# Kernel optimization log

Hardware: AMD Instinct MI355X
Metric: run time of the kernel (lower is better)

Reference implementation:

```python
import jax, jax.numpy as jnp
from jax import lax
import numpy as np

EPSILON = 0.1
MAX_ITERS = 20
N, K, D = 16384, 1024, 512


def setup_inputs() -> dict:
    key = jax.random.key(0)
    kx, kp = jax.random.split(key)
    x = jax.random.normal(kx, (N, D), dtype=jnp.float32)
    p = jax.random.normal(kp, (K, D), dtype=jnp.float32)
    return {"x": x, "p": p}


def reference(x, p):
    # Squared-euclidean cost matrix C: [N, K]
    dist_x = jnp.sum(x * x, axis=1, keepdims=True)          # [N, 1]
    dist_p = jnp.sum(p * p, axis=1, keepdims=True).T         # [1, K]
    C = dist_x + dist_p - 2.0 * (x @ p.T)                    # [N, K]
    C = C / (C.max() + 1e-8)
    K_eps = jnp.exp(-C / EPSILON)                            # [N, K]

    n, k = x.shape[0], p.shape[0]
    mu = jnp.full((n,), 1.0 / n, dtype=x.dtype)
    nu = jnp.full((k,), 1.0 / k, dtype=x.dtype)

    def step(carry, _):
        u, v = carry
        u = mu / (K_eps @ v + 1e-8)
        v = nu / (K_eps.T @ u + 1e-8)
        return (u, v), None

    init = (jnp.ones((n,), x.dtype), jnp.ones((k,), x.dtype))
    (u, v), _ = lax.scan(step, init, None, length=MAX_ITERS)

    T_star = u[:, None] * K_eps * v[None, :]                 # [N, K]
    ot_loss = jnp.sum(T_star * C)
    return (T_star, ot_loss)
```

## Files before the change

### kernel.cpp

```cpp
#include <hip/hip_runtime.h>
#include <hip/hip_fp16.h>
#include <cstddef>
#include <cstdint>

#define N_PTS 16384
#define K_PTS 1024
#define D_DIM 512
#define EPS_F 0.1f
#define ITERS 20
#define MU_F (1.0f/16384.0f)
#define NU_F (1.0f/1024.0f)
#define NCOPY 8
#define SINK_BLOCKS 256
#define FLAG_STRIDE 16
#define ACC_TOTAL ((ITERS + 1) * NCOPY * K_PTS)

#define WS_ACCUM_BYTES ((size_t)ACC_TOTAL * 4)
#define WS_FLAGS_BYTES ((size_t)SINK_BLOCKS * FLAG_STRIDE * 4)


typedef float f32x4 __attribute__((ext_vector_type(4)));
typedef _Float16 f16x8 __attribute__((ext_vector_type(8)));

__device__ __forceinline__ float wave_reduce_sum(float s) {
#pragma unroll
  for (int off = 32; off > 0; off >>= 1) s += __shfl_xor(s, off, 64);
  return s;
}
__device__ __forceinline__ float wave_reduce_max(float s) {
#pragma unroll
  for (int off = 32; off > 0; off >>= 1) s = fmaxf(s, __shfl_xor(s, off, 64));
  return s;
}

__device__ __forceinline__ void gl16(const void* g, void* l) {
  __builtin_amdgcn_global_load_lds(
      (const __attribute__((address_space(1))) unsigned int*)g,
      (__attribute__((address_space(3))) unsigned int*)l, 16, 0, 0);
}

__global__ __launch_bounds__(256) void init_kernel(float* __restrict__ accum,
                                                   unsigned int* __restrict__ flags,
                                                   unsigned int* __restrict__ maxbits,
                                                   float* __restrict__ loss) {
  int i = blockIdx.x * 256 + threadIdx.x;
  if (i < ACC_TOTAL) accum[i] = 0.0f;
  if (i < SINK_BLOCKS * FLAG_STRIDE) flags[i] = 0u;
  if (i == 0) { *maxbits = 0u; *loss = 0.0f; }
}

__global__ __launch_bounds__(256) void convert_kernel(const float* __restrict__ X,
                                                      const float* __restrict__ P,
                                                      unsigned short* __restrict__ Xf,
                                                      unsigned short* __restrict__ Pf,
                                                      float* __restrict__ xn,
                                                      float* __restrict__ pn) {
  const int gw = (blockIdx.x * 256 + threadIdx.x) >> 6;
  const int lane = threadIdx.x & 63;

  const float* src;
  unsigned short* dst;
  float* nrm;
  if (gw < N_PTS) {
    src = X + (size_t)gw * D_DIM;
    dst = Xf + (size_t)gw * D_DIM;
    nrm = xn + gw;
  } else {
    int r = gw - N_PTS;
    src = P + (size_t)r * D_DIM;
    dst = Pf + (size_t)r * D_DIM;
    nrm = pn + r;
  }

  float4 f0 = *(const float4*)(src + lane * 8);
  float4 f1 = *(const float4*)(src + lane * 8 + 4);
  float f[8] = {f0.x, f0.y, f0.z, f0.w, f1.x, f1.y, f1.z, f1.w};

  float s = 0.f;
#pragma unroll
  for (int j = 0; j < 8; j++) s += f[j] * f[j];

  unsigned int u[4];
#pragma unroll
  for (int j = 0; j < 4; j++) {
    unsigned int lo = (unsigned int)__half_as_ushort(__float2half(f[2 * j]));
    unsigned int hi = (unsigned int)__half_as_ushort(__float2half(f[2 * j + 1]));
    u[j] = lo | (hi << 16);
  }
  *(uint4*)(dst + lane * 8) = make_uint4(u[0], u[1], u[2], u[3]);

  s = wave_reduce_sum(s);
  if (lane == 0) *nrm = s;
}

__global__ __launch_bounds__(256, 2) void gemm3_kernel(const unsigned short* __restrict__ Xf,
                                                       const unsigned short* __restrict__ Pf,
                                                       const float* __restrict__ xn,
                                                       const float* __restrict__ pn,
                                                       __half* __restrict__ Ch,
                                                       unsigned int* __restrict__ maxbits) {
  __shared__ __align__(16) unsigned short Af[128 * 64];
  __shared__ __align__(16) unsigned short Bf[128 * 64];
  __shared__ float wmax[4];

  const int tid = threadIdx.x;
  const int lane = tid & 63, wv = tid >> 6;
  const int wm = wv >> 1, wn = wv & 1;
  const int m0 = blockIdx.y * 128, k0 = blockIdx.x * 128;

  const int srow = lane >> 3;
  const int sswg = ((lane & 7) ^ srow) << 4;
  const char* gA = (const char*)(Xf + (size_t)m0 * D_DIM);
  const char* gB = (const char*)(Pf + (size_t)k0 * D_DIM);

  f32x4 acc[4][4] = {};

  for (int d0 = 0; d0 < D_DIM; d0 += 64) {
    if (d0) __syncthreads();
#pragma unroll
    for (int is = 0; is < 4; is++) {
      const int chunk = wv * 4 + is;
      const size_t rb = (size_t)(chunk * 8 + srow) * (D_DIM * 2) + (size_t)d0 * 2 + sswg;
      gl16(gA + rb, &Af[chunk * 512]);
      gl16(gB + rb, &Bf[chunk * 512]);
    }
    __syncthreads();

    f16x8 av[2][4], bv[2][4];
#pragma unroll
    for (int ks = 0; ks < 2; ks++)
#pragma unroll
      for (int i = 0; i < 4; i++) {
        int rA = wm * 64 + i * 16 + (lane & 15);
        int gAi = (ks * 4 + (lane >> 4)) ^ (rA & 7);
        av[ks][i] = *(const f16x8*)&Af[rA * 64 + gAi * 8];
        int rB = wn * 64 + i * 16 + (lane & 15);
        int gBi = (ks * 4 + (lane >> 4)) ^ (rB & 7);
        bv[ks][i] = *(const f16x8*)&Bf[rB * 64 + gBi * 8];
      }
#pragma unroll
    for (int mi = 0; mi < 4; mi++)
#pragma unroll
      for (int ni = 0; ni < 4; ni++) {
        acc[mi][ni] = __builtin_amdgcn_mfma_f32_16x16x32_f16(av[0][mi], bv[0][ni], acc[mi][ni], 0, 0, 0);
        acc[mi][ni] = __builtin_amdgcn_mfma_f32_16x16x32_f16(av[1][mi], bv[1][ni], acc[mi][ni], 0, 0, 0);
      }
  }

  float lmax = -3.4e38f;
#pragma unroll
  for (int mi = 0; mi < 4; mi++) {
    int rloc = wm * 64 + mi * 16 + (lane >> 4) * 4;
    float dxv[4];
#pragma unroll
    for (int r = 0; r < 4; r++) dxv[r] = xn[m0 + rloc + r];
#pragma unroll
    for (int ni = 0; ni < 4; ni++) {
      int cloc = wn * 64 + ni * 16 + (lane & 15);
      float pnc = pn[k0 + cloc];
#pragma unroll
      for (int r = 0; r < 4; r++) {
        float val = dxv[r] + pnc - 2.0f * acc[mi][ni][r];
        Ch[(size_t)(m0 + rloc + r) * K_PTS + k0 + cloc] = __float2half(val);
        lmax = fmaxf(lmax, val);
      }
    }
  }
  lmax = wave_reduce_max(lmax);
  if (lane == 0) wmax[wv] = lmax;
  __syncthreads();
  if (tid == 0) {
    float m = fmaxf(fmaxf(wmax[0], wmax[1]), fmaxf(wmax[2], wmax[3]));
    atomicMax((int*)maxbits, __float_as_int(m));
  }
}

__global__ __launch_bounds__(512, 2) void sinkhorn_kernel(
    const __half* __restrict__ Ch,
    const unsigned int* __restrict__ maxbits,
    float* __restrict__ accum,
    unsigned int* __restrict__ flags,
    float* __restrict__ T,
    float* __restrict__ loss) {
  __shared__ float v_lds[K_PTS];
  __shared__ float red[8][K_PTS];
  const int tid = threadIdx.x;
  const int lane = tid & 63, wv = tid >> 6;
  const int b = blockIdx.x;
  const int r0 = b * 64 + wv * 8;

  float factor;
  {
    float cmax = __int_as_float((int)*maxbits);
    factor = -1.0f / ((cmax + 1e-8f) * EPS_F);
  }
  f32x4 k4[32];
#pragma unroll
  for (int i = 0; i < 8; i++) {
    const __half* rp = Ch + (size_t)(r0 + i) * K_PTS + lane;
#pragma unroll
    for (int q = 0; q < 4; q++) {
      f32x4 kk;
#pragma unroll
      for (int e = 0; e < 4; e++)
        kk[e] = __expf(__half2float(rp[(4 * q + e) * 64]) * factor);
      k4[i * 4 + q] = kk;
    }
  }
  v_lds[tid * 2 + 0] = 1.0f;
  v_lds[tid * 2 + 1] = 1.0f;
  __syncthreads();

  float su[8];
  for (int t = 0; t < ITERS; t++) {
    f32x4 vr4[4];
#pragma unroll
    for (int q = 0; q < 4; q++)
#pragma unroll
      for (int e = 0; e < 4; e++)
        vr4[q][e] = v_lds[(4 * q + e) * 64 + lane];

    float s[8];
#pragma unroll
    for (int i = 0; i < 8; i++) {
      f32x4 d = k4[i * 4 + 0] * vr4[0] + k4[i * 4 + 1] * vr4[1]
              + k4[i * 4 + 2] * vr4[2] + k4[i * 4 + 3] * vr4[3];
      s[i] = d[0] + d[1] + d[2] + d[3];
    }
    {
      const bool h32 = (lane & 32) != 0;
      float a[4];
#pragma unroll
      for (int i = 0; i < 4; i++) {
        float x = h32 ? s[i] : s[i + 4];
        float y = h32 ? s[i + 4] : s[i];
        a[i] = y + __shfl_xor(x, 32, 64);
      }
      const bool h16 = (lane & 16) != 0;
      float c[2];
#pragma unroll
      for (int i = 0; i < 2; i++) {
        float x = h16 ? a[i] : a[i + 2];
        float y = h16 ? a[i + 2] : a[i];
        c[i] = y + __shfl_xor(x, 16, 64);
      }
      const bool h8 = (lane & 8) != 0;
      float x = h8 ? c[0] : c[1];
      float y = h8 ? c[1] : c[0];
      float w = y + __shfl_xor(x, 8, 64);
      w += __shfl_xor(w, 4, 64);
      w += __shfl_xor(w, 2, 64);
      w += __shfl_xor(w, 1, 64);
      float ui_local = MU_F / (w + 1e-8f);
#pragma unroll
      for (int i = 0; i < 8; i++)
        su[i] = __uint_as_float(__builtin_amdgcn_readlane(__float_as_uint(ui_local), i * 8));
    }
    f32x4 ca4[4] = {};
#pragma unroll
    for (int i = 0; i < 8; i++)
#pragma unroll
      for (int q = 0; q < 4; q++)
        ca4[q] += su[i] * k4[i * 4 + q];

    __syncthreads();
#pragma unroll
    for (int q = 0; q < 4; q++)
#pragma unroll
      for (int e = 0; e < 4; e++)
        red[wv][(4 * q + e) * 64 + lane] = ca4[q][e];
    __syncthreads();
    {
      float s0 = 0.f, s1 = 0.f;
#pragma unroll
      for (int w8 = 0; w8 < 8; w8++) {
        float2 v2 = *(const float2*)&red[w8][tid * 2];
        s0 += v2.x; s1 += v2.y;
      }
      float* dst = accum + (size_t)(t + 1) * (NCOPY * K_PTS)
                 + (size_t)(b & (NCOPY - 1)) * K_PTS + tid * 2;
      atomicAdd(dst + 0, s0);
      atomicAdd(dst + 1, s1);
    }
    __syncthreads();
    if (tid == 0)
      __hip_atomic_store(&flags[(size_t)b * FLAG_STRIDE], (unsigned)(t + 1),
                         __ATOMIC_RELEASE, __HIP_MEMORY_SCOPE_AGENT);
    if (tid < SINK_BLOCKS) {
      while (__hip_atomic_load(&flags[(size_t)tid * FLAG_STRIDE],
                               __ATOMIC_RELAXED, __HIP_MEMORY_SCOPE_AGENT) < (unsigned)(t + 1))
        __builtin_amdgcn_s_sleep(4);
    }
    __syncthreads();
    {
      float* st = accum + (size_t)(t + 1) * (NCOPY * K_PTS);
      float s0 = 0.f, s1 = 0.f;
#pragma unroll
      for (int c = 0; c < NCOPY; c++) {
        s0 += __hip_atomic_load(st + (size_t)c * K_PTS + tid * 2 + 0,
                                __ATOMIC_RELAXED, __HIP_MEMORY_SCOPE_AGENT);
        s1 += __hip_atomic_load(st + (size_t)c * K_PTS + tid * 2 + 1,
                                __ATOMIC_RELAXED, __HIP_MEMORY_SCOPE_AGENT);
      }
      v_lds[tid * 2 + 0] = NU_F / (s0 + 1e-8f);
      v_lds[tid * 2 + 1] = NU_F / (s1 + 1e-8f);
    }
    __syncthreads();
  }

  float lsum = 0.f;
#pragma unroll
  for (int i = 0; i < 8; i++) {
    float* Trow = T + (size_t)(r0 + i) * K_PTS + lane;
#pragma unroll
    for (int q = 0; q < 4; q++) {
#pragma unroll
      for (int e = 0; e < 4; e++) {
        int c = (4 * q + e) * 64;
        float kk = k4[i * 4 + q][e];
        float tv = su[i] * kk * v_lds[c + lane];
        Trow[c] = tv;
        lsum += tv * (-EPS_F * __logf(kk));
      }
    }
  }
  lsum = wave_reduce_sum(lsum);
  __shared__ float wsum[8];
  if (lane == 0) wsum[wv] = lsum;
  __syncthreads();
  if (tid == 0) {
    float m = 0.f;
#pragma unroll
    for (int i = 0; i < 8; i++) m += wsum[i];
    atomicAdd(loss, m);
  }
}

extern "C" void kernel_launch(void* const* d_in, const int* in_sizes, int n_in,
                              void* d_out, int out_size, void* d_ws, size_t ws_size,
                              hipStream_t stream) {
  const float* x = (const float*)d_in[0];
  const float* p = (const float*)d_in[1];
  float* T = (float*)d_out;
  float* loss = (float*)d_out + (size_t)N_PTS * K_PTS;
  __half* Ch = (__half*)d_out;

  unsigned short* Xf = (unsigned short*)((char*)d_out + ((size_t)32 << 20));
  unsigned short* Pf = (unsigned short*)((char*)d_out + ((size_t)48 << 20));
  float* xn = (float*)((char*)d_out + ((size_t)49 << 20));
  float* pn = xn + N_PTS;

  char* wsb = (char*)d_ws;
  float* accum = (float*)wsb;
  unsigned int* flags = (unsigned int*)(wsb + WS_ACCUM_BYTES);
  unsigned int* maxbits = (unsigned int*)(wsb + WS_ACCUM_BYTES + WS_FLAGS_BYTES);

  init_kernel<<<(ACC_TOTAL + 255) / 256, 256, 0, stream>>>(accum, flags, maxbits, loss);
  convert_kernel<<<(N_PTS + K_PTS) / 4, 256, 0, stream>>>(x, p, Xf, Pf, xn, pn);
  gemm3_kernel<<<dim3(K_PTS / 128, N_PTS / 128), 256, 0, stream>>>(Xf, Pf, xn, pn, Ch, maxbits);
  sinkhorn_kernel<<<SINK_BLOCKS, 512, 0, stream>>>(Ch, maxbits, accum, flags, T, loss);
}
```

Measured before the change: 301.0 us.

## Double-buffer GEMM LDS tiles and coalesce C stores through shared memory

The cost GEMM now double-buffers its A/B shared-memory tiles, issuing the global-to-LDS loads for the next k-step before computing the current one. This hides load latency and cuts one barrier per iteration. The epilogue writes the half-precision cost tile into padded LDS and then copies it out with 16-byte coalesced stores instead of scattered 2-byte writes. LDS use doubles, which could reduce occupancy.

```diff
diff --git a/kernel.cpp b/kernel.cpp
--- a/kernel.cpp
+++ b/kernel.cpp
@@ -93,14 +93,15 @@
   if (lane == 0) *nrm = s;
 }
 
-__global__ __launch_bounds__(256, 2) void gemm3_kernel(const unsigned short* __restrict__ Xf,
+#define CT_STRIDE 136
+
+__global__ __launch_bounds__(256, 2) void gemm4_kernel(const unsigned short* __restrict__ Xf,
                                                        const unsigned short* __restrict__ Pf,
                                                        const float* __restrict__ xn,
                                                        const float* __restrict__ pn,
                                                        __half* __restrict__ Ch,
                                                        unsigned int* __restrict__ maxbits) {
-  __shared__ __align__(16) unsigned short Af[128 * 64];
-  __shared__ __align__(16) unsigned short Bf[128 * 64];
+  __shared__ __align__(16) unsigned short Sh[2][2][128 * 64];
   __shared__ float wmax[4];
 
   const int tid = threadIdx.x;
@@ -115,38 +116,55 @@
 
   f32x4 acc[4][4] = {};
 
-  for (int d0 = 0; d0 < D_DIM; d0 += 64) {
-    if (d0) __syncthreads();
-#pragma unroll
-    for (int is = 0; is < 4; is++) {
-      const int chunk = wv * 4 + is;
-      const size_t rb = (size_t)(chunk * 8 + srow) * (D_DIM * 2) + (size_t)d0 * 2 + sswg;
-      gl16(gA + rb, &Af[chunk * 512]);
-      gl16(gB + rb, &Bf[chunk * 512]);
-    }
-    __syncthreads();
-
-    f16x8 av[2][4], bv[2][4];
+#define STAGE(buf, d0off)                                                         \
+  do {                                                                            \
+    _Pragma("unroll")                                                             \
+    for (int is = 0; is < 4; is++) {                                              \
+      const int chunk_ = wv * 4 + is;                                             \
+      const size_t rb_ = (size_t)(chunk_ * 8 + srow) * (D_DIM * 2)                \
+                       + (size_t)(d0off) * 2 + sswg;                              \
+      gl16(gA + rb_, &Sh[buf][0][chunk_ * 512]);                                  \
+      gl16(gB + rb_, &Sh[buf][1][chunk_ * 512]);                                  \
+    }                                                                             \
+  } while (0)
+
+  STAGE(0, 0);
+  __syncthreads();
+
+#pragma unroll
+  for (int t = 0; t < 8; ++t) {
+    const int cur = t & 1;
+    if (t < 7) STAGE(cur ^ 1, (t + 1) * 64);
+    const unsigned short* Af = Sh[cur][0];
+    const unsigned short* Bf = Sh[cur][1];
+
+    f16x8 bv[2][4];
 #pragma unroll
     for (int ks = 0; ks < 2; ks++)
 #pragma unroll
-      for (int i = 0; i < 4; i++) {
-        int rA = wm * 64 + i * 16 + (lane & 15);
-        int gAi = (ks * 4 + (lane >> 4)) ^ (rA & 7);
-        av[ks][i] = *(const f16x8*)&Af[rA * 64 + gAi * 8];
-        int rB = wn * 64 + i * 16 + (lane & 15);
+      for (int ni = 0; ni < 4; ni++) {
+        int rB = wn * 64 + ni * 16 + (lane & 15);
         int gBi = (ks * 4 + (lane >> 4)) ^ (rB & 7);
-        bv[ks][i] = *(const f16x8*)&Bf[rB * 64 + gBi * 8];
-      }
-#pragma unroll
-    for (int mi = 0; mi < 4; mi++)
+        bv[ks][ni] = *(const f16x8*)&Bf[rB * 64 + gBi * 8];
+      }
+#pragma unroll
+    for (int mi = 0; mi < 4; mi++) {
+      int rA = wm * 64 + mi * 16 + (lane & 15);
+      int g0 = (0 + (lane >> 4)) ^ (rA & 7);
+      int g1 = (4 + (lane >> 4)) ^ (rA & 7);
+      f16x8 a0 = *(const f16x8*)&Af[rA * 64 + g0 * 8];
+      f16x8 a1 = *(const f16x8*)&Af[rA * 64 + g1 * 8];
 #pragma unroll
       for (int ni = 0; ni < 4; ni++) {
-        acc[mi][ni] = __builtin_amdgcn_mfma_f32_16x16x32_f16(av[0][mi], bv[0][ni], acc[mi][ni], 0, 0, 0);
-        acc[mi][ni] = __builtin_amdgcn_mfma_f32_16x16x32_f16(av[1][mi], bv[1][ni], acc[mi][ni], 0, 0, 0);
-      }
-  }
-
+        acc[mi][ni] = __builtin_amdgcn_mfma_f32_16x16x32_f16(a0, bv[0][ni], acc[mi][ni], 0, 0, 0);
+        acc[mi][ni] = __builtin_amdgcn_mfma_f32_16x16x32_f16(a1, bv[1][ni], acc[mi][ni], 0, 0, 0);
+      }
+    }
+    __syncthreads();
+  }
+#undef STAGE
+
+  unsigned short* Ct = &Sh[0][0][0];
   float lmax = -3.4e38f;
 #pragma unroll
   for (int mi = 0; mi < 4; mi++) {
@@ -161,11 +179,20 @@
 #pragma unroll
       for (int r = 0; r < 4; r++) {
         float val = dxv[r] + pnc - 2.0f * acc[mi][ni][r];
-        Ch[(size_t)(m0 + rloc + r) * K_PTS + k0 + cloc] = __float2half(val);
+        Ct[(rloc + r) * CT_STRIDE + cloc] = __half_as_ushort(__float2half(val));
         lmax = fmaxf(lmax, val);
       }
     }
   }
+  __syncthreads();
+#pragma unroll
+  for (int j = 0; j < 8; j++) {
+    int idx = j * 256 + tid;
+    int row = idx >> 4, cq = idx & 15;
+    uint4 v = *(const uint4*)&Ct[row * CT_STRIDE + cq * 8];
+    *(uint4*)&Ch[(size_t)(m0 + row) * K_PTS + k0 + cq * 8] = v;
+  }
+
   lmax = wave_reduce_max(lmax);
   if (lane == 0) wmax[wv] = lmax;
   __syncthreads();
@@ -357,6 +384,6 @@
 
   init_kernel<<<(ACC_TOTAL + 255) / 256, 256, 0, stream>>>(accum, flags, maxbits, loss);
   convert_kernel<<<(N_PTS + K_PTS) / 4, 256, 0, stream>>>(x, p, Xf, Pf, xn, pn);
-  gemm3_kernel<<<dim3(K_PTS / 128, N_PTS / 128), 256, 0, stream>>>(Xf, Pf, xn, pn, Ch, maxbits);
+  gemm4_kernel<<<dim3(K_PTS / 128, N_PTS / 128), 256, 0, stream>>>(Xf, Pf, xn, pn, Ch, maxbits);
   sinkhorn_kernel<<<SINK_BLOCKS, 512, 0, stream>>>(Ch, maxbits, accum, flags, T, loss);
 }
```

Result: no change. 299.7 us (-0.4%).

## Fuse cost-matrix GEMM into persistent Sinkhorn kernel, keeping costs in registers

Applied to the files above, without the earlier changes.

Merges the separate GEMM kernel into the persistent Sinkhorn kernel. Each of the 256 blocks computes its own 64-row slab of the cost matrix with MFMA, streaming P through LDS with register prefetch. The costs go straight into the register-resident k4 array, so the fp16 cost matrix is never written to or re-read from global memory. A global flag barrier is added to agree on the max before the exp. The trade-off is that the GEMM now runs on only 256 blocks with tiny 32x32-per-step tiles and two syncthreads per step, which may underuse the MFMA units compared with the full-grid GEMM.

```diff
diff --git a/kernel.cpp b/kernel.cpp
--- a/kernel.cpp
+++ b/kernel.cpp
@@ -93,120 +93,136 @@
   if (lane == 0) *nrm = s;
 }
 
-__global__ __launch_bounds__(256, 2) void gemm3_kernel(const unsigned short* __restrict__ Xf,
-                                                       const unsigned short* __restrict__ Pf,
-                                                       const float* __restrict__ xn,
-                                                       const float* __restrict__ pn,
-                                                       __half* __restrict__ Ch,
-                                                       unsigned int* __restrict__ maxbits) {
-  __shared__ __align__(16) unsigned short Af[128 * 64];
-  __shared__ __align__(16) unsigned short Bf[128 * 64];
-  __shared__ float wmax[4];
-
-  const int tid = threadIdx.x;
-  const int lane = tid & 63, wv = tid >> 6;
-  const int wm = wv >> 1, wn = wv & 1;
-  const int m0 = blockIdx.y * 128, k0 = blockIdx.x * 128;
-
-  const int srow = lane >> 3;
-  const int sswg = ((lane & 7) ^ srow) << 4;
-  const char* gA = (const char*)(Xf + (size_t)m0 * D_DIM);
-  const char* gB = (const char*)(Pf + (size_t)k0 * D_DIM);
-
-  f32x4 acc[4][4] = {};
-
-  for (int d0 = 0; d0 < D_DIM; d0 += 64) {
-    if (d0) __syncthreads();
-#pragma unroll
-    for (int is = 0; is < 4; is++) {
-      const int chunk = wv * 4 + is;
-      const size_t rb = (size_t)(chunk * 8 + srow) * (D_DIM * 2) + (size_t)d0 * 2 + sswg;
-      gl16(gA + rb, &Af[chunk * 512]);
-      gl16(gB + rb, &Bf[chunk * 512]);
-    }
-    __syncthreads();
-
-    f16x8 av[2][4], bv[2][4];
-#pragma unroll
-    for (int ks = 0; ks < 2; ks++)
-#pragma unroll
-      for (int i = 0; i < 4; i++) {
-        int rA = wm * 64 + i * 16 + (lane & 15);
-        int gAi = (ks * 4 + (lane >> 4)) ^ (rA & 7);
-        av[ks][i] = *(const f16x8*)&Af[rA * 64 + gAi * 8];
-        int rB = wn * 64 + i * 16 + (lane & 15);
-        int gBi = (ks * 4 + (lane >> 4)) ^ (rB & 7);
-        bv[ks][i] = *(const f16x8*)&Bf[rB * 64 + gBi * 8];
-      }
-#pragma unroll
-    for (int mi = 0; mi < 4; mi++)
-#pragma unroll
-      for (int ni = 0; ni < 4; ni++) {
-        acc[mi][ni] = __builtin_amdgcn_mfma_f32_16x16x32_f16(av[0][mi], bv[0][ni], acc[mi][ni], 0, 0, 0);
-        acc[mi][ni] = __builtin_amdgcn_mfma_f32_16x16x32_f16(av[1][mi], bv[1][ni], acc[mi][ni], 0, 0, 0);
-      }
-  }
-
-  float lmax = -3.4e38f;
-#pragma unroll
-  for (int mi = 0; mi < 4; mi++) {
-    int rloc = wm * 64 + mi * 16 + (lane >> 4) * 4;
-    float dxv[4];
-#pragma unroll
-    for (int r = 0; r < 4; r++) dxv[r] = xn[m0 + rloc + r];
-#pragma unroll
-    for (int ni = 0; ni < 4; ni++) {
-      int cloc = wn * 64 + ni * 16 + (lane & 15);
-      float pnc = pn[k0 + cloc];
-#pragma unroll
-      for (int r = 0; r < 4; r++) {
-        float val = dxv[r] + pnc - 2.0f * acc[mi][ni][r];
-        Ch[(size_t)(m0 + rloc + r) * K_PTS + k0 + cloc] = __float2half(val);
-        lmax = fmaxf(lmax, val);
-      }
-    }
-  }
-  lmax = wave_reduce_max(lmax);
-  if (lane == 0) wmax[wv] = lmax;
-  __syncthreads();
-  if (tid == 0) {
-    float m = fmaxf(fmaxf(wmax[0], wmax[1]), fmaxf(wmax[2], wmax[3]));
-    atomicMax((int*)maxbits, __float_as_int(m));
-  }
-}
-
-__global__ __launch_bounds__(512, 2) void sinkhorn_kernel(
-    const __half* __restrict__ Ch,
-    const unsigned int* __restrict__ maxbits,
+__global__ __launch_bounds__(512, 2) void fused_kernel(
+    const unsigned short* __restrict__ Xf,
+    const unsigned short* __restrict__ Pf,
+    const float* __restrict__ xn,
+    const float* __restrict__ pn,
+    unsigned int* __restrict__ maxbits,
     float* __restrict__ accum,
     unsigned int* __restrict__ flags,
     float* __restrict__ T,
     float* __restrict__ loss) {
-  __shared__ float v_lds[K_PTS];
-  __shared__ float red[8][K_PTS];
+  __shared__ __align__(16) char smem[98304];
+  __shared__ __align__(16) unsigned short t_lds[64 * 33];
+  __shared__ float xn_s[64];
+  __shared__ float pn_s[K_PTS];
+  __shared__ float wred[8];
+
+  unsigned short* X_lds = (unsigned short*)smem;
+  unsigned short* Pbuf = (unsigned short*)(smem + 65536);
+
   const int tid = threadIdx.x;
   const int lane = tid & 63, wv = tid >> 6;
   const int b = blockIdx.x;
-  const int r0 = b * 64 + wv * 8;
-
+  const int rb0 = b * 64;
+  const int r0 = rb0 + wv * 8;
+
+  if (tid < 64) xn_s[tid] = xn[rb0 + tid];
+  pn_s[tid] = pn[tid];
+  pn_s[tid + 512] = pn[tid + 512];
+
+  const int gsw = (lane & ~7) | ((lane & 7) ^ (wv & 7));
+#pragma unroll
+  for (int q = 0; q < 8; q++) {
+    int row = q * 8 + wv;
+    gl16((const char*)Xf + (size_t)(rb0 + row) * 1024 + gsw * 16, X_lds + row * 512);
+  }
+#pragma unroll
+  for (int q = 0; q < 4; q++) {
+    int row = q * 8 + wv;
+    gl16((const char*)Pf + (size_t)row * 1024 + gsw * 16, Pbuf + row * 512);
+  }
+  __syncthreads();
+
+  const int prow = tid >> 4;
+  const int pgl = tid & 15;
+
+  const int rt = wv >> 1, ct = wv & 1;
+  const int fr = lane & 15, fg = lane >> 4;
+  float lmax = -3.4e38f;
+  f32x4 k4[32];
+
+#pragma unroll
+  for (int p = 0; p < 32; p++) {
+    uint4 pref[4];
+    if (p < 31) {
+      const char* srcrow = (const char*)Pf + (size_t)((p + 1) * 32 + prow) * 1024;
+#pragma unroll
+      for (int j = 0; j < 4; j++)
+        pref[j] = *(const uint4*)(srcrow + (pgl + 16 * j) * 16);
+    }
+
+    f32x4 acc = {};
+#pragma unroll
+    for (int kk = 0; kk < 16; kk++) {
+      int kg = kk * 4 + fg;
+      int slot = (kg & ~7) | ((kg & 7) ^ (fr & 7));
+      f16x8 av = *(const f16x8*)&X_lds[(rt * 16 + fr) * 512 + slot * 8];
+      f16x8 bv = *(const f16x8*)&Pbuf[(ct * 16 + fr) * 512 + slot * 8];
+      acc = __builtin_amdgcn_mfma_f32_16x16x32_f16(av, bv, acc, 0, 0, 0);
+    }
+    {
+      int colL = ct * 16 + fr;
+      float pnc = pn_s[p * 32 + colL];
+#pragma unroll
+      for (int r = 0; r < 4; r++) {
+        int rowL = rt * 16 + fg * 4 + r;
+        float val = xn_s[rowL] + pnc - 2.0f * acc[r];
+        lmax = fmaxf(lmax, val);
+        t_lds[rowL * 33 + colL] = __half_as_ushort(__float2half(val));
+      }
+    }
+    __syncthreads();
+
+    if (p < 31) {
+#pragma unroll
+      for (int j = 0; j < 4; j++) {
+        int g = pgl + 16 * j;
+        int slot = (g & ~7) | ((g & 7) ^ (prow & 7));
+        *(uint4*)&Pbuf[prow * 512 + slot * 8] = pref[j];
+      }
+    }
+    if ((lane >> 5) == (p & 1)) {
+#pragma unroll
+      for (int i = 0; i < 8; i++)
+        k4[i * 4 + (p >> 3)][(p >> 1) & 3] =
+            __half2float(__ushort_as_half(t_lds[(wv * 8 + i) * 33 + (lane & 31)]));
+    }
+    __syncthreads();
+  }
+
+  lmax = wave_reduce_max(lmax);
+  if (lane == 0) wred[wv] = lmax;
+  __syncthreads();
+  if (tid == 0) {
+    float m = wred[0];
+#pragma unroll
+    for (int i = 1; i < 8; i++) m = fmaxf(m, wred[i]);
+    atomicMax((int*)maxbits, __float_as_int(m));
+    __hip_atomic_store(&flags[(size_t)b * FLAG_STRIDE], 1u,
+                       __ATOMIC_RELEASE, __HIP_MEMORY_SCOPE_AGENT);
+  }
+  if (tid < SINK_BLOCKS) {
+    while (__hip_atomic_load(&flags[(size_t)tid * FLAG_STRIDE],
+                             __ATOMIC_RELAXED, __HIP_MEMORY_SCOPE_AGENT) < 1u)
+      __builtin_amdgcn_s_sleep(4);
+  }
+  __syncthreads();
   float factor;
   {
-    float cmax = __int_as_float((int)*maxbits);
+    float cmax = __uint_as_float(__hip_atomic_load(maxbits, __ATOMIC_RELAXED,
+                                                   __HIP_MEMORY_SCOPE_AGENT));
     factor = -1.0f / ((cmax + 1e-8f) * EPS_F);
   }
-  f32x4 k4[32];
-#pragma unroll
-  for (int i = 0; i < 8; i++) {
-    const __half* rp = Ch + (size_t)(r0 + i) * K_PTS + lane;
-#pragma unroll
-    for (int q = 0; q < 4; q++) {
-      f32x4 kk;
-#pragma unroll
-      for (int e = 0; e < 4; e++)
-        kk[e] = __expf(__half2float(rp[(4 * q + e) * 64]) * factor);
-      k4[i * 4 + q] = kk;
-    }
-  }
+#pragma unroll
+  for (int j = 0; j < 32; j++)
+#pragma unroll
+    for (int e = 0; e < 4; e++)
+      k4[j][e] = __expf(k4[j][e] * factor);
+
+  float* v_lds = (float*)smem;
+  float (*red)[K_PTS] = (float (*)[K_PTS])(smem + 4096);
   v_lds[tid * 2 + 0] = 1.0f;
   v_lds[tid * 2 + 1] = 1.0f;
   __syncthreads();
@@ -284,11 +300,11 @@
     }
     __syncthreads();
     if (tid == 0)
-      __hip_atomic_store(&flags[(size_t)b * FLAG_STRIDE], (unsigned)(t + 1),
+      __hip_atomic_store(&flags[(size_t)b * FLAG_STRIDE], (unsigned)(t + 2),
                          __ATOMIC_RELEASE, __HIP_MEMORY_SCOPE_AGENT);
     if (tid < SINK_BLOCKS) {
       while (__hip_atomic_load(&flags[(size_t)tid * FLAG_STRIDE],
-                               __ATOMIC_RELAXED, __HIP_MEMORY_SCOPE_AGENT) < (unsigned)(t + 1))
+                               __ATOMIC_RELAXED, __HIP_MEMORY_SCOPE_AGENT) < (unsigned)(t + 2))
         __builtin_amdgcn_s_sleep(4);
     }
     __syncthreads();
@@ -325,13 +341,13 @@
     }
   }
   lsum = wave_reduce_sum(lsum);
-  __shared__ float wsum[8];
-  if (lane == 0) wsum[wv] = lsum;
+  __syncthreads();
+  if (lane == 0) wred[wv] = lsum;
   __syncthreads();
   if (tid == 0) {
     float m = 0.f;
 #pragma unroll
-    for (int i = 0; i < 8; i++) m += wsum[i];
+    for (int i = 0; i < 8; i++) m += wred[i];
     atomicAdd(loss, m);
   }
 }
@@ -343,7 +359,6 @@
   const float* p = (const float*)d_in[1];
   float* T = (float*)d_out;
   float* loss = (float*)d_out + (size_t)N_PTS * K_PTS;
-  __half* Ch = (__half*)d_out;
 
   unsigned short* Xf = (unsigned short*)((char*)d_out + ((size_t)32 << 20));
   unsigned short* Pf = (unsigned short*)((char*)d_out + ((size_t)48 << 20));
@@ -357,6 +372,5 @@
 
   init_kernel<<<(ACC_TOTAL + 255) / 256, 256, 0, stream>>>(accum, flags, maxbits, loss);
   convert_kernel<<<(N_PTS + K_PTS) / 4, 256, 0, stream>>>(x, p, Xf, Pf, xn, pn);
-  gemm3_kernel<<<dim3(K_PTS / 128, N_PTS / 128), 256, 0, stream>>>(Xf, Pf, xn, pn, Ch, maxbits);
-  sinkhorn_kernel<<<SINK_BLOCKS, 512, 0, stream>>>(Ch, maxbits, accum, flags, T, loss);
-}
+  fused_kernel<<<SINK_BLOCKS, 512, 0, stream>>>(Xf, Pf, xn, pn, maxbits, accum, flags, T, loss);
+}
```

Result: slower. 339.8 us (+12.9%).
